# Performance work log

Measured on AMD Instinct MI355X. Metric: run time of the kernel, lower is better.

Reference implementation:

```python
import jax, jax.numpy as jnp
import numpy as np

B, N, DIM, H = 4, 1024, 384, 12
EPS = 1e-6


def setup_inputs() -> dict:
    key = jax.random.key(0)
    ks = jax.random.split(key, 5)
    return {
        "x": jax.random.normal(ks[0], (B, N, DIM), dtype=jnp.float32),
        "w_qkv": jax.random.normal(ks[1], (DIM, 3 * DIM), dtype=jnp.float32) * 0.05,
        "w_out": jax.random.normal(ks[2], (DIM, DIM), dtype=jnp.float32) * 0.05,
        "b_out": jax.random.normal(ks[3], (DIM,), dtype=jnp.float32) * 0.05,
        "toeplitz_w": jax.random.normal(ks[4], (2 * N - 1,), dtype=jnp.float32),
    }


def reference(x, w_qkv, w_out, b_out, toeplitz_w):
    b, n, c = x.shape
    d = c // H
    qkv = x @ w_qkv                                   # [B,N,3C]
    q, k, v = jnp.split(qkv, 3, axis=-1)
    def heads(t):
        return t.reshape(b, n, H, d).transpose(0, 2, 1, 3)  # [B,H,N,d]
    q, k, v = heads(q), heads(k), heads(v)
    q = jax.nn.relu(q) + EPS
    k = jax.nn.relu(k) + EPS
    # outer product kv signal: [B,H,N,d,d]
    kv = k[..., :, None] * v[..., None, :]
    kv_flat = kv.reshape(b * H, n, d * d)
    k_flat = k.reshape(b * H, n, d)
    combined = jnp.concatenate([kv_flat, k_flat], axis=-1)   # [BH,N,d^2+d]
    fft_len = 2 * n
    sig_f = jnp.fft.rfft(combined, n=fft_len, axis=1)        # [BH,N+1,d^2+d] complex
    w_pad = jnp.zeros(fft_len, dtype=x.dtype).at[: 2 * n - 1].set(toeplitz_w)
    w_rolled = jnp.roll(w_pad, -(n - 1))
    w_f = jnp.fft.rfft(w_rolled, n=fft_len)                  # [N+1]
    out_f = sig_f * w_f[None, :, None]
    out_t = jnp.fft.irfft(out_f, n=fft_len, axis=1)[:, :n, :]  # [BH,N,d^2+d]
    kv_conv = out_t[:, :, : d * d].reshape(b, H, n, d, d)
    k_conv = out_t[:, :, d * d:].reshape(b, H, n, d)
    num = jnp.einsum('bhnd,bhndc->bhnc', q, kv_conv)
    den = jnp.einsum('bhnd,bhnd->bhn', q, k_conv)[..., None] + EPS
    out = (num / den).transpose(0, 2, 1, 3).reshape(b, n, c)
    return out @ w_out.T + b_out
```

## Files before the change

### kernel.cpp

```cpp
#include <hip/hip_runtime.h>

#define EPS 1e-6f


__global__ __launch_bounds__(256) void qkv_gemm(const float* __restrict__ x,
                                                const float* __restrict__ w,
                                                float* __restrict__ qw,
                                                float* __restrict__ kw,
                                                float* __restrict__ vw) {
    __shared__ float As[32][68];
    __shared__ float Bs[32][68];
    const int t = threadIdx.x;
    const int m0 = blockIdx.y * 64;
    const int c0 = blockIdx.x * 64;
    const int tx = t & 15, ty = t >> 4;

    float acc[4][4];
#pragma unroll
    for (int i = 0; i < 4; i++)
#pragma unroll
        for (int j = 0; j < 4; j++) acc[i][j] = 0.f;

    for (int k0 = 0; k0 < 384; k0 += 32) {
        __syncthreads();
#pragma unroll
        for (int l = 0; l < 2; l++) {
            int idx = t * 2 + l;
            int r = idx >> 3, c4 = (idx & 7) * 4;
            float4 a = *(const float4*)(x + (size_t)(m0 + r) * 384 + k0 + c4);
            As[c4 + 0][r] = a.x;
            As[c4 + 1][r] = a.y;
            As[c4 + 2][r] = a.z;
            As[c4 + 3][r] = a.w;
        }
#pragma unroll
        for (int l = 0; l < 2; l++) {
            int idx = t * 2 + l;
            int kr = idx >> 4, cc = (idx & 15) * 4;
            *(float4*)&Bs[kr][cc] = *(const float4*)(w + (size_t)(k0 + kr) * 1152 + c0 + cc);
        }
        __syncthreads();
#pragma unroll
        for (int kk = 0; kk < 32; kk++) {
            float4 a = *(float4*)&As[kk][ty * 4];
            float4 bb = *(float4*)&Bs[kk][tx * 4];
            float av[4] = {a.x, a.y, a.z, a.w};
            float bv[4] = {bb.x, bb.y, bb.z, bb.w};
#pragma unroll
            for (int i = 0; i < 4; i++)
#pragma unroll
                for (int j = 0; j < 4; j++) acc[i][j] += av[i] * bv[j];
        }
    }
    const int sec = (c0 + tx * 4) / 384;
    float* dst = (sec == 0) ? qw : (sec == 1) ? kw : vw;
    const int cc0 = c0 + tx * 4 - sec * 384;
    const int h = cc0 >> 5, dd = cc0 & 31;
#pragma unroll
    for (int i = 0; i < 4; i++) {
        int row = m0 + ty * 4 + i;
        int b = row >> 10, n = row & 1023;
        float4 o;
        if (sec < 2) {
            o.x = fmaxf(acc[i][0], 0.f) + EPS;
            o.y = fmaxf(acc[i][1], 0.f) + EPS;
            o.z = fmaxf(acc[i][2], 0.f) + EPS;
            o.w = fmaxf(acc[i][3], 0.f) + EPS;
        } else {
            o = make_float4(acc[i][0], acc[i][1], acc[i][2], acc[i][3]);
        }
        *(float4*)(dst + (size_t)((b * 12 + h) * 1024 + n) * 32 + dd) = o;
    }
}

__global__ __launch_bounds__(256) void toep_attn(const float* __restrict__ q,
                                                 const float* __restrict__ k,
                                                 const float* __restrict__ v,
                                                 const float* __restrict__ tw,
                                                 float* __restrict__ op) {
    const int t = threadIdx.x;
    const int n0 = blockIdx.x * 64;
    const int bh = blockIdx.y;
    const int b = bh / 12, h = bh % 12;
    __shared__ float Qt[32][68];
    __shared__ float Kt[32][68];
    __shared__ double Vd[64][34];
    __shared__ float Ss[64][68];
    __shared__ float Ts[128];

    const float* qb = q + (size_t)bh * 32768;
    const float* kb = k + (size_t)bh * 32768;
    const float* vb = v + (size_t)bh * 32768;

#pragma unroll
    for (int l = 0; l < 2; l++) {
        int idx = t * 2 + l;
        int r = idx >> 3, c4 = (idx & 7) * 4;
        float4 a = *(const float4*)(qb + (size_t)(n0 + r) * 32 + c4);
        Qt[c4 + 0][r] = a.x;
        Qt[c4 + 1][r] = a.y;
        Qt[c4 + 2][r] = a.z;
        Qt[c4 + 3][r] = a.w;
    }

    float4 kreg[2], vreg[2];
#pragma unroll
    for (int l = 0; l < 2; l++) {
        int idx = t * 2 + l;
        int r = idx >> 3, c4 = (idx & 7) * 4;
        kreg[l] = *(const float4*)(kb + (size_t)r * 32 + c4);
        vreg[l] = *(const float4*)(vb + idx * 4);
    }
#pragma unroll
    for (int l = 0; l < 2; l++) {
        int idx = t * 2 + l;
        int r = idx >> 3, c4 = (idx & 7) * 4;
        Kt[c4 + 0][r] = kreg[l].x;
        Kt[c4 + 1][r] = kreg[l].y;
        Kt[c4 + 2][r] = kreg[l].z;
        Kt[c4 + 3][r] = kreg[l].w;
        double2 d0 = {(double)vreg[l].x, (double)vreg[l].y};
        double2 d1 = {(double)vreg[l].z, (double)vreg[l].w};
        *(double2*)&Vd[r][c4] = d0;
        *(double2*)&Vd[r][c4 + 2] = d1;
    }
    if (t < 127) Ts[t] = tw[n0 + 960 + t];
    __syncthreads();

    const int sx = t & 15, sy = t >> 4;
    const int pr = t >> 2;
    const int pc = (t & 3) * 8;
    double num[8] = {0, 0, 0, 0, 0, 0, 0, 0};
    double den = 0.0;

    for (int tt = 0; tt < 16; tt++) {
        const int m0 = tt * 64;
        if (tt < 15) {
#pragma unroll
            for (int l = 0; l < 2; l++) {
                int idx = t * 2 + l;
                int r = idx >> 3, c4 = (idx & 7) * 4;
                kreg[l] = *(const float4*)(kb + (size_t)(m0 + 64 + r) * 32 + c4);
                vreg[l] = *(const float4*)(vb + (size_t)(m0 + 64) * 32 + idx * 4);
            }
        }

        float acc[4][4];
#pragma unroll
        for (int i = 0; i < 4; i++)
#pragma unroll
            for (int j = 0; j < 4; j++) acc[i][j] = 0.f;
#pragma unroll
        for (int kk = 0; kk < 32; kk++) {
            float4 a = *(float4*)&Qt[kk][sy * 4];
            float4 bb = *(float4*)&Kt[kk][sx * 4];
            float av[4] = {a.x, a.y, a.z, a.w};
            float bv[4] = {bb.x, bb.y, bb.z, bb.w};
#pragma unroll
            for (int i = 0; i < 4; i++)
#pragma unroll
                for (int j = 0; j < 4; j++) acc[i][j] += av[i] * bv[j];
        }
#pragma unroll
        for (int i = 0; i < 4; i++) {
            int r = sy * 4 + i;
            float4 srow;
            srow.x = acc[i][0] * Ts[r - sx * 4 + 63];
            srow.y = acc[i][1] * Ts[r - sx * 4 + 62];
            srow.z = acc[i][2] * Ts[r - sx * 4 + 61];
            srow.w = acc[i][3] * Ts[r - sx * 4 + 60];
            *(float4*)&Ss[r][sx * 4] = srow;
        }
        __syncthreads();

        if (tt < 15) {
#pragma unroll
            for (int l = 0; l < 2; l++) {
                int idx = t * 2 + l;
                int r = idx >> 3, c4 = (idx & 7) * 4;
                Kt[c4 + 0][r] = kreg[l].x;
                Kt[c4 + 1][r] = kreg[l].y;
                Kt[c4 + 2][r] = kreg[l].z;
                Kt[c4 + 3][r] = kreg[l].w;
            }
            if (t < 127) Ts[t] = tw[n0 - (m0 + 64) + 960 + t];
        }

#pragma unroll 4
        for (int m = 0; m < 64; m++) {
            double s = (double)Ss[pr][m];
            double2 va  = *(double2*)&Vd[m][pc];
            double2 vb2 = *(double2*)&Vd[m][pc + 2];
            double2 vc  = *(double2*)&Vd[m][pc + 4];
            double2 vd2 = *(double2*)&Vd[m][pc + 6];
            den += s;
            num[0] += s * va.x;  num[1] += s * va.y;
            num[2] += s * vb2.x; num[3] += s * vb2.y;
            num[4] += s * vc.x;  num[5] += s * vc.y;
            num[6] += s * vd2.x; num[7] += s * vd2.y;
        }
        __syncthreads();
        if (tt < 15) {
#pragma unroll
            for (int l = 0; l < 2; l++) {
                int idx = t * 2 + l;
                int r = idx >> 3, c4 = (idx & 7) * 4;
                double2 d0 = {(double)vreg[l].x, (double)vreg[l].y};
                double2 d1 = {(double)vreg[l].z, (double)vreg[l].w};
                *(double2*)&Vd[r][c4] = d0;
                *(double2*)&Vd[r][c4 + 2] = d1;
            }
        }
    }
    double inv = 1.0 / (den + (double)EPS);
    float* o = op + (size_t)((b * 1024) + n0 + pr) * 384 + h * 32 + pc;
    float4 o0 = {(float)(num[0] * inv), (float)(num[1] * inv),
                 (float)(num[2] * inv), (float)(num[3] * inv)};
    float4 o1 = {(float)(num[4] * inv), (float)(num[5] * inv),
                 (float)(num[6] * inv), (float)(num[7] * inv)};
    *(float4*)o = o0;
    *(float4*)(o + 4) = o1;
}

__global__ __launch_bounds__(256) void out_gemm(const float* __restrict__ a,
                                                const float* __restrict__ w,
                                                const float* __restrict__ bias,
                                                float* __restrict__ out) {
    __shared__ float As[32][68];
    __shared__ float Bs[32][68];
    const int t = threadIdx.x;
    const int m0 = blockIdx.y * 64;
    const int c0 = blockIdx.x * 64;
    const int tx = t & 15, ty = t >> 4;

    float acc[4][4];
#pragma unroll
    for (int i = 0; i < 4; i++)
#pragma unroll
        for (int j = 0; j < 4; j++) acc[i][j] = 0.f;

    for (int k0 = 0; k0 < 384; k0 += 32) {
        __syncthreads();
#pragma unroll
        for (int l = 0; l < 2; l++) {
            int idx = t * 2 + l;
            int r = idx >> 3, c4 = (idx & 7) * 4;
            float4 av = *(const float4*)(a + (size_t)(m0 + r) * 384 + k0 + c4);
            As[c4 + 0][r] = av.x;
            As[c4 + 1][r] = av.y;
            As[c4 + 2][r] = av.z;
            As[c4 + 3][r] = av.w;
        }
#pragma unroll
        for (int l = 0; l < 2; l++) {
            int idx = t * 2 + l;
            int r = idx >> 3, c4 = (idx & 7) * 4;
            float4 wv = *(const float4*)(w + (size_t)(c0 + r) * 384 + k0 + c4);
            Bs[c4 + 0][r] = wv.x;
            Bs[c4 + 1][r] = wv.y;
            Bs[c4 + 2][r] = wv.z;
            Bs[c4 + 3][r] = wv.w;
        }
        __syncthreads();
#pragma unroll
        for (int kk = 0; kk < 32; kk++) {
            float4 a4 = *(float4*)&As[kk][ty * 4];
            float4 b4 = *(float4*)&Bs[kk][tx * 4];
            float av[4] = {a4.x, a4.y, a4.z, a4.w};
            float bv[4] = {b4.x, b4.y, b4.z, b4.w};
#pragma unroll
            for (int i = 0; i < 4; i++)
#pragma unroll
                for (int j = 0; j < 4; j++) acc[i][j] += av[i] * bv[j];
        }
    }
    const int col = c0 + tx * 4;
    float4 bb = *(const float4*)(bias + col);
#pragma unroll
    for (int i = 0; i < 4; i++) {
        int row = m0 + ty * 4 + i;
        float4 o = {acc[i][0] + bb.x, acc[i][1] + bb.y,
                    acc[i][2] + bb.z, acc[i][3] + bb.w};
        *(float4*)(out + (size_t)row * 384 + col) = o;
    }
}

extern "C" void kernel_launch(void* const* d_in, const int* in_sizes, int n_in,
                              void* d_out, int out_size, void* d_ws, size_t ws_size,
                              hipStream_t stream) {
    const float* x     = (const float*)d_in[0];
    const float* w_qkv = (const float*)d_in[1];
    const float* w_out = (const float*)d_in[2];
    const float* b_out = (const float*)d_in[3];
    const float* tw    = (const float*)d_in[4];
    float* out = (float*)d_out;

    float* qw = (float*)d_ws;
    float* kw = qw + 1572864;
    float* vw = kw + 1572864;
    float* op = vw + 1572864;

    qkv_gemm<<<dim3(18, 64), 256, 0, stream>>>(x, w_qkv, qw, kw, vw);
    toep_attn<<<dim3(16, 48), 256, 0, stream>>>(qw, kw, vw, tw, op);
    out_gemm<<<dim3(6, 64), 256, 0, stream>>>(op, w_out, b_out, out);
}
```

Before: 313.7 us.

## Halve query tile in Toeplitz attention kernel and store V as float in LDS

New measurement: 333.6 us. 1.06x slower.

```diff
diff --git a/kernel.cpp b/kernel.cpp
--- a/kernel.cpp
+++ b/kernel.cpp
@@ -79,23 +79,21 @@
                                                  const float* __restrict__ tw,
                                                  float* __restrict__ op) {
     const int t = threadIdx.x;
-    const int n0 = blockIdx.x * 64;
+    const int n0 = blockIdx.x * 32;
     const int bh = blockIdx.y;
     const int b = bh / 12, h = bh % 12;
-    __shared__ float Qt[32][68];
+    __shared__ float Qt[32][36];
     __shared__ float Kt[32][68];
-    __shared__ double Vd[64][34];
-    __shared__ float Ss[64][68];
+    __shared__ float Vs[64][36];
+    __shared__ float Ss[32][68];
     __shared__ float Ts[128];
 
     const float* qb = q + (size_t)bh * 32768;
     const float* kb = k + (size_t)bh * 32768;
     const float* vb = v + (size_t)bh * 32768;
 
-#pragma unroll
-    for (int l = 0; l < 2; l++) {
-        int idx = t * 2 + l;
-        int r = idx >> 3, c4 = (idx & 7) * 4;
+    {
+        int r = t >> 3, c4 = (t & 7) * 4;
         float4 a = *(const float4*)(qb + (size_t)(n0 + r) * 32 + c4);
         Qt[c4 + 0][r] = a.x;
         Qt[c4 + 1][r] = a.y;
@@ -119,18 +117,15 @@
         Kt[c4 + 1][r] = kreg[l].y;
         Kt[c4 + 2][r] = kreg[l].z;
         Kt[c4 + 3][r] = kreg[l].w;
-        double2 d0 = {(double)vreg[l].x, (double)vreg[l].y};
-        double2 d1 = {(double)vreg[l].z, (double)vreg[l].w};
-        *(double2*)&Vd[r][c4] = d0;
-        *(double2*)&Vd[r][c4 + 2] = d1;
-    }
-    if (t < 127) Ts[t] = tw[n0 + 960 + t];
+        *(float4*)&Vs[r][c4] = vreg[l];
+    }
+    if (t < 95) Ts[t] = tw[n0 + 960 + t];
     __syncthreads();
 
-    const int sx = t & 15, sy = t >> 4;
-    const int pr = t >> 2;
-    const int pc = (t & 3) * 8;
-    double num[8] = {0, 0, 0, 0, 0, 0, 0, 0};
+    const int sy = t >> 4, sx = t & 15;
+    const int pr = t >> 3;
+    const int pc = (t & 7) * 4;
+    double num[4] = {0, 0, 0, 0};
     double den = 0.0;
 
     for (int tt = 0; tt < 16; tt++) {
@@ -145,25 +140,25 @@
             }
         }
 
-        float acc[4][4];
-#pragma unroll
-        for (int i = 0; i < 4; i++)
+        float acc[2][4];
+#pragma unroll
+        for (int i = 0; i < 2; i++)
 #pragma unroll
             for (int j = 0; j < 4; j++) acc[i][j] = 0.f;
 #pragma unroll
         for (int kk = 0; kk < 32; kk++) {
-            float4 a = *(float4*)&Qt[kk][sy * 4];
-            float4 bb = *(float4*)&Kt[kk][sx * 4];
-            float av[4] = {a.x, a.y, a.z, a.w};
-            float bv[4] = {bb.x, bb.y, bb.z, bb.w};
-#pragma unroll
-            for (int i = 0; i < 4; i++)
+            float2 qa = *(float2*)&Qt[kk][sy * 2];
+            float4 kb4 = *(float4*)&Kt[kk][sx * 4];
+            float av[2] = {qa.x, qa.y};
+            float bv[4] = {kb4.x, kb4.y, kb4.z, kb4.w};
+#pragma unroll
+            for (int i = 0; i < 2; i++)
 #pragma unroll
                 for (int j = 0; j < 4; j++) acc[i][j] += av[i] * bv[j];
         }
 #pragma unroll
-        for (int i = 0; i < 4; i++) {
-            int r = sy * 4 + i;
+        for (int i = 0; i < 2; i++) {
+            int r = sy * 2 + i;
             float4 srow;
             srow.x = acc[i][0] * Ts[r - sx * 4 + 63];
             srow.y = acc[i][1] * Ts[r - sx * 4 + 62];
@@ -183,21 +178,18 @@
                 Kt[c4 + 2][r] = kreg[l].z;
                 Kt[c4 + 3][r] = kreg[l].w;
             }
-            if (t < 127) Ts[t] = tw[n0 - (m0 + 64) + 960 + t];
+            if (t < 95) Ts[t] = tw[n0 - (m0 + 64) + 960 + t];
         }
 
 #pragma unroll 4
         for (int m = 0; m < 64; m++) {
             double s = (double)Ss[pr][m];
-            double2 va  = *(double2*)&Vd[m][pc];
-            double2 vb2 = *(double2*)&Vd[m][pc + 2];
-            double2 vc  = *(double2*)&Vd[m][pc + 4];
-            double2 vd2 = *(double2*)&Vd[m][pc + 6];
+            float4 vv = *(float4*)&Vs[m][pc];
             den += s;
-            num[0] += s * va.x;  num[1] += s * va.y;
-            num[2] += s * vb2.x; num[3] += s * vb2.y;
-            num[4] += s * vc.x;  num[5] += s * vc.y;
-            num[6] += s * vd2.x; num[7] += s * vd2.y;
+            num[0] += s * (double)vv.x;
+            num[1] += s * (double)vv.y;
+            num[2] += s * (double)vv.z;
+            num[3] += s * (double)vv.w;
         }
         __syncthreads();
         if (tt < 15) {
@@ -205,10 +197,7 @@
             for (int l = 0; l < 2; l++) {
                 int idx = t * 2 + l;
                 int r = idx >> 3, c4 = (idx & 7) * 4;
-                double2 d0 = {(double)vreg[l].x, (double)vreg[l].y};
-                double2 d1 = {(double)vreg[l].z, (double)vreg[l].w};
-                *(double2*)&Vd[r][c4] = d0;
-                *(double2*)&Vd[r][c4 + 2] = d1;
+                *(float4*)&Vs[r][c4] = vreg[l];
             }
         }
     }
@@ -216,10 +205,7 @@
     float* o = op + (size_t)((b * 1024) + n0 + pr) * 384 + h * 32 + pc;
     float4 o0 = {(float)(num[0] * inv), (float)(num[1] * inv),
                  (float)(num[2] * inv), (float)(num[3] * inv)};
-    float4 o1 = {(float)(num[4] * inv), (float)(num[5] * inv),
-                 (float)(num[6] * inv), (float)(num[7] * inv)};
     *(float4*)o = o0;
-    *(float4*)(o + 4) = o1;
 }
 
 __global__ __launch_bounds__(256) void out_gemm(const float* __restrict__ a,
@@ -301,6 +287,6 @@
     float* op = vw + 1572864;
 
     qkv_gemm<<<dim3(18, 64), 256, 0, stream>>>(x, w_qkv, qw, kw, vw);
-    toep_attn<<<dim3(16, 48), 256, 0, stream>>>(qw, kw, vw, tw, op);
+    toep_attn<<<dim3(32, 48), 256, 0, stream>>>(qw, kw, vw, tw, op);
     out_gemm<<<dim3(6, 64), 256, 0, stream>>>(op, w_out, b_out, out);
 }
```

## Register-tile the S·V accumulation and store V as float in shared memory

Applied to the files above, without the earlier changes.

Result: slower. 324.4 us (+3.4%).

```diff
diff --git a/kernel.cpp b/kernel.cpp
--- a/kernel.cpp
+++ b/kernel.cpp
@@ -84,8 +84,8 @@
     const int b = bh / 12, h = bh % 12;
     __shared__ float Qt[32][68];
     __shared__ float Kt[32][68];
-    __shared__ double Vd[64][34];
-    __shared__ float Ss[64][68];
+    __shared__ float Vs[64][36];
+    __shared__ float St[64][68];
     __shared__ float Ts[128];
 
     const float* qb = q + (size_t)bh * 32768;
@@ -109,7 +109,7 @@
         int idx = t * 2 + l;
         int r = idx >> 3, c4 = (idx & 7) * 4;
         kreg[l] = *(const float4*)(kb + (size_t)r * 32 + c4);
-        vreg[l] = *(const float4*)(vb + idx * 4);
+        vreg[l] = *(const float4*)(vb + (size_t)r * 32 + c4);
     }
 #pragma unroll
     for (int l = 0; l < 2; l++) {
@@ -119,19 +119,23 @@
         Kt[c4 + 1][r] = kreg[l].y;
         Kt[c4 + 2][r] = kreg[l].z;
         Kt[c4 + 3][r] = kreg[l].w;
-        double2 d0 = {(double)vreg[l].x, (double)vreg[l].y};
-        double2 d1 = {(double)vreg[l].z, (double)vreg[l].w};
-        *(double2*)&Vd[r][c4] = d0;
-        *(double2*)&Vd[r][c4 + 2] = d1;
+        *(float4*)&Vs[r][c4] = vreg[l];
     }
     if (t < 127) Ts[t] = tw[n0 + 960 + t];
     __syncthreads();
 
-    const int sx = t & 15, sy = t >> 4;
-    const int pr = t >> 2;
-    const int pc = (t & 3) * 8;
-    double num[8] = {0, 0, 0, 0, 0, 0, 0, 0};
-    double den = 0.0;
+    const int rgrp = t & 15;
+    const int mgrp = t >> 4;
+    const int mhalf = t & 1;
+    const int rgrp2 = (t >> 1) & 15;
+    const int cgrp = t >> 5;
+
+    double num[4][4];
+#pragma unroll
+    for (int i = 0; i < 4; i++)
+#pragma unroll
+        for (int j = 0; j < 4; j++) num[i][j] = 0.0;
+    double den[4] = {0.0, 0.0, 0.0, 0.0};
 
     for (int tt = 0; tt < 16; tt++) {
         const int m0 = tt * 64;
@@ -141,7 +145,7 @@
                 int idx = t * 2 + l;
                 int r = idx >> 3, c4 = (idx & 7) * 4;
                 kreg[l] = *(const float4*)(kb + (size_t)(m0 + 64 + r) * 32 + c4);
-                vreg[l] = *(const float4*)(vb + (size_t)(m0 + 64) * 32 + idx * 4);
+                vreg[l] = *(const float4*)(vb + (size_t)(m0 + 64 + r) * 32 + c4);
             }
         }
 
@@ -152,24 +156,25 @@
             for (int j = 0; j < 4; j++) acc[i][j] = 0.f;
 #pragma unroll
         for (int kk = 0; kk < 32; kk++) {
-            float4 a = *(float4*)&Qt[kk][sy * 4];
-            float4 bb = *(float4*)&Kt[kk][sx * 4];
-            float av[4] = {a.x, a.y, a.z, a.w};
-            float bv[4] = {bb.x, bb.y, bb.z, bb.w};
+            float4 qv = *(float4*)&Qt[kk][rgrp * 4];
+            float4 kv = *(float4*)&Kt[kk][mgrp * 4];
+            float av[4] = {qv.x, qv.y, qv.z, qv.w};
+            float bv[4] = {kv.x, kv.y, kv.z, kv.w};
 #pragma unroll
             for (int i = 0; i < 4; i++)
 #pragma unroll
                 for (int j = 0; j < 4; j++) acc[i][j] += av[i] * bv[j];
         }
 #pragma unroll
-        for (int i = 0; i < 4; i++) {
-            int r = sy * 4 + i;
+        for (int j = 0; j < 4; j++) {
+            int m = mgrp * 4 + j;
+            int tb = rgrp * 4 - m + 63;
             float4 srow;
-            srow.x = acc[i][0] * Ts[r - sx * 4 + 63];
-            srow.y = acc[i][1] * Ts[r - sx * 4 + 62];
-            srow.z = acc[i][2] * Ts[r - sx * 4 + 61];
-            srow.w = acc[i][3] * Ts[r - sx * 4 + 60];
-            *(float4*)&Ss[r][sx * 4] = srow;
+            srow.x = acc[0][j] * Ts[tb + 0];
+            srow.y = acc[1][j] * Ts[tb + 1];
+            srow.z = acc[2][j] * Ts[tb + 2];
+            srow.w = acc[3][j] * Ts[tb + 3];
+            *(float4*)&St[m][rgrp * 4] = srow;
         }
         __syncthreads();
 
@@ -187,17 +192,18 @@
         }
 
 #pragma unroll 4
-        for (int m = 0; m < 64; m++) {
-            double s = (double)Ss[pr][m];
-            double2 va  = *(double2*)&Vd[m][pc];
-            double2 vb2 = *(double2*)&Vd[m][pc + 2];
-            double2 vc  = *(double2*)&Vd[m][pc + 4];
-            double2 vd2 = *(double2*)&Vd[m][pc + 6];
-            den += s;
-            num[0] += s * va.x;  num[1] += s * va.y;
-            num[2] += s * vb2.x; num[3] += s * vb2.y;
-            num[4] += s * vc.x;  num[5] += s * vc.y;
-            num[6] += s * vd2.x; num[7] += s * vd2.y;
+        for (int m2 = 0; m2 < 32; m2++) {
+            int m = 2 * m2 + mhalf;
+            float4 s4 = *(float4*)&St[m][rgrp2 * 4];
+            float4 v4 = *(float4*)&Vs[m][cgrp * 4];
+            double sd[4] = {(double)s4.x, (double)s4.y, (double)s4.z, (double)s4.w};
+            double vd[4] = {(double)v4.x, (double)v4.y, (double)v4.z, (double)v4.w};
+#pragma unroll
+            for (int i = 0; i < 4; i++) {
+                den[i] += sd[i];
+#pragma unroll
+                for (int j = 0; j < 4; j++) num[i][j] += sd[i] * vd[j];
+            }
         }
         __syncthreads();
         if (tt < 15) {
@@ -205,21 +211,26 @@
             for (int l = 0; l < 2; l++) {
                 int idx = t * 2 + l;
                 int r = idx >> 3, c4 = (idx & 7) * 4;
-                double2 d0 = {(double)vreg[l].x, (double)vreg[l].y};
-                double2 d1 = {(double)vreg[l].z, (double)vreg[l].w};
-                *(double2*)&Vd[r][c4] = d0;
-                *(double2*)&Vd[r][c4 + 2] = d1;
+                *(float4*)&Vs[r][c4] = vreg[l];
             }
         }
     }
-    double inv = 1.0 / (den + (double)EPS);
-    float* o = op + (size_t)((b * 1024) + n0 + pr) * 384 + h * 32 + pc;
-    float4 o0 = {(float)(num[0] * inv), (float)(num[1] * inv),
-                 (float)(num[2] * inv), (float)(num[3] * inv)};
-    float4 o1 = {(float)(num[4] * inv), (float)(num[5] * inv),
-                 (float)(num[6] * inv), (float)(num[7] * inv)};
-    *(float4*)o = o0;
-    *(float4*)(o + 4) = o1;
+
+#pragma unroll
+    for (int i = 0; i < 4; i++) {
+        den[i] += __shfl_xor(den[i], 1);
+#pragma unroll
+        for (int j = 0; j < 4; j++) num[i][j] += __shfl_xor(num[i][j], 1);
+    }
+#pragma unroll
+    for (int rr = 0; rr < 2; rr++) {
+        int i = 2 * mhalf + rr;
+        double inv = 1.0 / (den[i] + (double)EPS);
+        int row = n0 + rgrp2 * 4 + i;
+        float4 o = {(float)(num[i][0] * inv), (float)(num[i][1] * inv),
+                    (float)(num[i][2] * inv), (float)(num[i][3] * inv)};
+        *(float4*)(op + (size_t)(b * 1024 + row) * 384 + h * 32 + cgrp * 4) = o;
+    }
 }
 
 __global__ __launch_bounds__(256) void out_gemm(const float* __restrict__ a,
```
